# Performance work log

Measured on AMD Instinct MI355X. Metric: run time of the kernel, lower is better.

The kernel has to match this reference:

```python
import jax, jax.numpy as jnp
import numpy as np

EPS = 1e-12

def _normalize(v):
    n = jnp.linalg.norm(v, axis=-1, keepdims=True)
    return v / jnp.maximum(n, EPS)

def _bgs(J):
    # J: [b, N, D, 3, 2] -> rotation matrices R [b, N, D, 3, 3]
    b1 = _normalize(J[..., :, 0])
    a2 = J[..., :, 1]
    dot = jnp.sum(b1 * a2, axis=-1, keepdims=True)
    b2 = _normalize(a2 - dot * b1)
    b3 = jnp.cross(b1, b2)
    return jnp.stack([b1, b2, b3], axis=-1)  # columns b1,b2,b3

def setup_inputs() -> dict:
    key = jax.random.key(0)
    k1, k2, k3, k4, k5 = jax.random.split(key, 5)
    B, N, D, OUT = 16, 4096, 64, 64
    X = jax.random.normal(k1, (B, N, D, 3), dtype=jnp.float32)
    J = jax.random.normal(k2, (B, N, D, 3, 2), dtype=jnp.float32)
    A = jax.random.normal(k3, (OUT, D), dtype=jnp.float32)
    Bm = jax.random.normal(k4, (OUT, D), dtype=jnp.float32)
    C = jax.random.normal(k5, (OUT, D), dtype=jnp.float32)
    return {"X": X, "J": J, "A": A, "Bm": Bm, "C": C}

def reference(X, J, A, Bm, C):
    R = _bgs(J)  # [b, N, D, 3, 3]
    # RT_i . X == column i of R dotted with X -> scalar per channel
    RTX = jnp.einsum('bndij,bndi->bndj', R, X)  # [b, N, D, 3], j-th entry = RT_j X
    rt0 = RTX[..., 0:1]
    rt1 = RTX[..., 1:2]
    rt2 = RTX[..., 2:3]
    col0 = R[..., :, 0]
    col1 = R[..., :, 1]
    col2 = R[..., :, 2]
    # a_term (after adding b_term, as in original forward)
    a_term = col1 * rt1 + col2 * rt2 + col2 * rt1 - col1 * rt2  # [b, N, D, 3]
    c_term = col0 * rt0
    Y = jnp.einsum('fe,bnei->bnfi', A, a_term) + jnp.einsum('fe,bnei->bnfi', C, c_term)
    Y = jnp.einsum('fe,bnei->bnfi', Bm, Y)
    return Y
```

## Files before the change

### kernel.cpp

```cpp
#include <hip/hip_runtime.h>


typedef __bf16 bf16x8 __attribute__((ext_vector_type(8)));
typedef float floatx4 __attribute__((ext_vector_type(4)));

#define RSW 68

__global__ __launch_bounds__(256) void prep_kernel(const float* __restrict__ A,
                                                   const float* __restrict__ Bm,
                                                   const float* __restrict__ C,
                                                   __bf16* __restrict__ acat) {
    int tid = blockIdx.x * 256 + threadIdx.x;
    int f = tid >> 6;
    int e = tid & 63;
    float m = 0.f, m2 = 0.f;
    #pragma unroll 8
    for (int k = 0; k < 64; ++k) {
        float b = Bm[f * 64 + k];
        m  = fmaf(b, A[k * 64 + e], m);
        m2 = fmaf(b, C[k * 64 + e], m2);
    }
    acat[f * 128 + 2 * e]     = (__bf16)m;
    acat[f * 128 + 2 * e + 1] = (__bf16)m2;
}

static __device__ __forceinline__ unsigned pk(float a, float c) {
    unsigned short ua = __builtin_bit_cast(unsigned short, (__bf16)a);
    unsigned short uc = __builtin_bit_cast(unsigned short, (__bf16)c);
    return ((unsigned)uc << 16) | ua;
}

__global__ __launch_bounds__(256, 3) void main_kernel(const float* __restrict__ X,
                                                      const float* __restrict__ J,
                                                      const __bf16* __restrict__ acat,
                                                      float* __restrict__ out) {
    __shared__ __align__(16) float buf[4][3120];

    const int wave = threadIdx.x >> 6;
    const int lane = threadIdx.x & 63;
    const int l15  = lane & 15;
    const int quad = lane >> 4;
    const int pbase = blockIdx.x * 16 + wave * 4;

    float* stg = buf[wave];

    {
        const floatx4* jg = (const floatx4*)(J + (size_t)pbase * 384);
        const floatx4* xg = (const floatx4*)(X + (size_t)pbase * 192);
        floatx4 jt[6], xt[3];
        #pragma unroll
        for (int t = 0; t < 6; ++t) jt[t] = jg[t * 64 + lane];
        #pragma unroll
        for (int t = 0; t < 3; ++t) xt[t] = xg[t * 64 + lane];
        floatx4* sj = (floatx4*)stg;
        floatx4* sx = (floatx4*)(stg + 1536);
        #pragma unroll
        for (int t = 0; t < 6; ++t) sj[t * 64 + lane] = jt[t];
        #pragma unroll
        for (int t = 0; t < 3; ++t) sx[t * 64 + lane] = xt[t];
    }

    __asm__ volatile("s_waitcnt lgkmcnt(0)" ::: "memory");

    unsigned* zw = (unsigned*)(stg + 2304);

    #pragma unroll
    for (int pi = 0; pi < 4; ++pi) {
        const float* jst = stg + pi * 384 + lane * 6;
        float2 ja = *(const float2*)(jst);
        float2 jb = *(const float2*)(jst + 2);
        float2 jc = *(const float2*)(jst + 4);
        const float* xst = stg + 1536 + pi * 192 + lane * 3;
        float xx = xst[0], xy = xst[1], xz = xst[2];

        float a0x = ja.x, a0y = jb.x, a0z = jc.x;
        float a1x = ja.y, a1y = jb.y, a1z = jc.y;

        float n0 = sqrtf(a0x * a0x + a0y * a0y + a0z * a0z);
        float r0 = 1.0f / fmaxf(n0, 1e-12f);
        float b1x = a0x * r0, b1y = a0y * r0, b1z = a0z * r0;

        float d  = b1x * a1x + b1y * a1y + b1z * a1z;
        float ux = a1x - d * b1x, uy = a1y - d * b1y, uz = a1z - d * b1z;
        float n2 = sqrtf(ux * ux + uy * uy + uz * uz);
        float r2 = 1.0f / fmaxf(n2, 1e-12f);
        float b2x = ux * r2, b2y = uy * r2, b2z = uz * r2;

        float b3x = b1y * b2z - b1z * b2y;
        float b3y = b1z * b2x - b1x * b2z;
        float b3z = b1x * b2y - b1y * b2x;

        float rt0 = b1x * xx + b1y * xy + b1z * xz;
        float rt1 = b2x * xx + b2y * xy + b2z * xz;
        float rt2 = b3x * xx + b3y * xy + b3z * xz;

        float s = rt1 - rt2, t = rt1 + rt2;

        unsigned* zr = zw + (pi * 3) * RSW;
        zr[lane]           = pk(b2x * s + b3x * t, b1x * rt0);
        zr[RSW + lane]     = pk(b2y * s + b3y * t, b1y * rt0);
        zr[2 * RSW + lane] = pk(b2z * s + b3z * t, b1z * rt0);
    }

    bf16x8 afrag[4][4];
    #pragma unroll
    for (int mt = 0; mt < 4; ++mt)
        #pragma unroll
        for (int kc = 0; kc < 4; ++kc)
            afrag[mt][kc] = *(const bf16x8*)(acat + (mt * 16 + l15) * 128 + kc * 32 + quad * 8);

    __asm__ volatile("s_waitcnt lgkmcnt(0)" ::: "memory");

    floatx4 acc[4];
    #pragma unroll
    for (int mt = 0; mt < 4; ++mt) acc[mt] = (floatx4){0.f, 0.f, 0.f, 0.f};

    int row = l15 > 11 ? 11 : l15;
    #pragma unroll
    for (int kc = 0; kc < 4; ++kc) {
        bf16x8 b = *(const bf16x8*)((const __bf16*)zw + row * 136 + kc * 32 + quad * 8);
        #pragma unroll
        for (int mt = 0; mt < 4; ++mt)
            acc[mt] = __builtin_amdgcn_mfma_f32_16x16x32_bf16(afrag[mt][kc], b, acc[mt], 0, 0, 0);
    }

    __asm__ volatile("s_waitcnt lgkmcnt(0)" ::: "memory");

    float* dl = stg;
    #pragma unroll
    for (int mt = 0; mt < 4; ++mt) {
        int n = l15;
        if (n < 12) {
            int pl = (n * 21846) >> 16;
            int i  = n - pl * 3;
            float* dst = dl + pl * 196 + i;
            #pragma unroll
            for (int r = 0; r < 4; ++r) {
                int f = mt * 16 + quad * 4 + r;
                dst[f * 3] = acc[mt][r];
            }
        }
    }

    __asm__ volatile("s_waitcnt lgkmcnt(0)" ::: "memory");

    floatx4* og = (floatx4*)(out + (size_t)pbase * 192);
    #pragma unroll
    for (int t = 0; t < 3; ++t) {
        int g  = t * 64 + lane;
        int pg = (g * 1366) >> 16;
        int o  = g - pg * 48;
        og[g] = *(const floatx4*)(dl + pg * 196 + o * 4);
    }
}

extern "C" void kernel_launch(void* const* d_in, const int* in_sizes, int n_in,
                              void* d_out, int out_size, void* d_ws, size_t ws_size,
                              hipStream_t stream) {
    const float* X  = (const float*)d_in[0];
    const float* J  = (const float*)d_in[1];
    const float* A  = (const float*)d_in[2];
    const float* Bm = (const float*)d_in[3];
    const float* C  = (const float*)d_in[4];
    float* out = (float*)d_out;
    __bf16* acat = (__bf16*)d_ws;

    prep_kernel<<<16, 256, 0, stream>>>(A, Bm, C, acat);

    main_kernel<<<4096, 256, 0, stream>>>(X, J, acat, out);
}
```

Before: 209.2 us.

## Use direct global-to-LDS loads, persistent loop over tiles, smaller LDS footprint

Replaces the register-staged global loads of J and X with global_load_lds builtins that write straight into shared memory. The kernel becomes persistent: each wave handles four tiles in a loop, and the grid shrinks by a factor of four, so the B-matrix fragments are loaded once per wave and reused across tiles. Per-wave LDS drops (buffers overlap), which allows four blocks per CU. The risk is that with no prefetch, each iteration's loads are serialized behind the compute, and overlapping the buffers within a wave needs careful ordering.

```diff
diff --git a/kernel.cpp b/kernel.cpp
--- a/kernel.cpp
+++ b/kernel.cpp
@@ -5,6 +5,14 @@
 typedef float floatx4 __attribute__((ext_vector_type(4)));
 
 #define RSW 68
+#define WLDS 2320
+
+typedef const __attribute__((address_space(1))) unsigned guint;
+typedef __attribute__((address_space(3))) unsigned suint;
+
+static __device__ __forceinline__ void load16(const float* g, float* l) {
+    __builtin_amdgcn_global_load_lds((guint*)g, (suint*)l, 16, 0, 0);
+}
 
 __global__ __launch_bounds__(256) void prep_kernel(const float* __restrict__ A,
                                                    const float* __restrict__ Bm,
@@ -30,77 +38,17 @@
     return ((unsigned)uc << 16) | ua;
 }
 
-__global__ __launch_bounds__(256, 3) void main_kernel(const float* __restrict__ X,
+__global__ __launch_bounds__(256, 4) void main_kernel(const float* __restrict__ X,
                                                       const float* __restrict__ J,
                                                       const __bf16* __restrict__ acat,
                                                       float* __restrict__ out) {
-    __shared__ __align__(16) float buf[4][3120];
+    __shared__ __align__(16) float buf[4][WLDS];
 
     const int wave = threadIdx.x >> 6;
     const int lane = threadIdx.x & 63;
     const int l15  = lane & 15;
     const int quad = lane >> 4;
-    const int pbase = blockIdx.x * 16 + wave * 4;
-
     float* stg = buf[wave];
-
-    {
-        const floatx4* jg = (const floatx4*)(J + (size_t)pbase * 384);
-        const floatx4* xg = (const floatx4*)(X + (size_t)pbase * 192);
-        floatx4 jt[6], xt[3];
-        #pragma unroll
-        for (int t = 0; t < 6; ++t) jt[t] = jg[t * 64 + lane];
-        #pragma unroll
-        for (int t = 0; t < 3; ++t) xt[t] = xg[t * 64 + lane];
-        floatx4* sj = (floatx4*)stg;
-        floatx4* sx = (floatx4*)(stg + 1536);
-        #pragma unroll
-        for (int t = 0; t < 6; ++t) sj[t * 64 + lane] = jt[t];
-        #pragma unroll
-        for (int t = 0; t < 3; ++t) sx[t * 64 + lane] = xt[t];
-    }
-
-    __asm__ volatile("s_waitcnt lgkmcnt(0)" ::: "memory");
-
-    unsigned* zw = (unsigned*)(stg + 2304);
-
-    #pragma unroll
-    for (int pi = 0; pi < 4; ++pi) {
-        const float* jst = stg + pi * 384 + lane * 6;
-        float2 ja = *(const float2*)(jst);
-        float2 jb = *(const float2*)(jst + 2);
-        float2 jc = *(const float2*)(jst + 4);
-        const float* xst = stg + 1536 + pi * 192 + lane * 3;
-        float xx = xst[0], xy = xst[1], xz = xst[2];
-
-        float a0x = ja.x, a0y = jb.x, a0z = jc.x;
-        float a1x = ja.y, a1y = jb.y, a1z = jc.y;
-
-        float n0 = sqrtf(a0x * a0x + a0y * a0y + a0z * a0z);
-        float r0 = 1.0f / fmaxf(n0, 1e-12f);
-        float b1x = a0x * r0, b1y = a0y * r0, b1z = a0z * r0;
-
-        float d  = b1x * a1x + b1y * a1y + b1z * a1z;
-        float ux = a1x - d * b1x, uy = a1y - d * b1y, uz = a1z - d * b1z;
-        float n2 = sqrtf(ux * ux + uy * uy + uz * uz);
-        float r2 = 1.0f / fmaxf(n2, 1e-12f);
-        float b2x = ux * r2, b2y = uy * r2, b2z = uz * r2;
-
-        float b3x = b1y * b2z - b1z * b2y;
-        float b3y = b1z * b2x - b1x * b2z;
-        float b3z = b1x * b2y - b1y * b2x;
-
-        float rt0 = b1x * xx + b1y * xy + b1z * xz;
-        float rt1 = b2x * xx + b2y * xy + b2z * xz;
-        float rt2 = b3x * xx + b3y * xy + b3z * xz;
-
-        float s = rt1 - rt2, t = rt1 + rt2;
-
-        unsigned* zr = zw + (pi * 3) * RSW;
-        zr[lane]           = pk(b2x * s + b3x * t, b1x * rt0);
-        zr[RSW + lane]     = pk(b2y * s + b3y * t, b1y * rt0);
-        zr[2 * RSW + lane] = pk(b2z * s + b3z * t, b1z * rt0);
-    }
 
     bf16x8 afrag[4][4];
     #pragma unroll
@@ -109,48 +57,101 @@
         for (int kc = 0; kc < 4; ++kc)
             afrag[mt][kc] = *(const bf16x8*)(acat + (mt * 16 + l15) * 128 + kc * 32 + quad * 8);
 
-    __asm__ volatile("s_waitcnt lgkmcnt(0)" ::: "memory");
+    #pragma unroll 1
+    for (int it = 0; it < 4; ++it) {
+        const int tile = it * 4096 + blockIdx.x * 4 + wave;
+        const size_t pbase = (size_t)tile * 4;
 
-    floatx4 acc[4];
-    #pragma unroll
-    for (int mt = 0; mt < 4; ++mt) acc[mt] = (floatx4){0.f, 0.f, 0.f, 0.f};
+        const float* jg = J + pbase * 384;
+        const float* xg = X + pbase * 192;
+        #pragma unroll
+        for (int t = 0; t < 6; ++t) load16(jg + (t * 64 + lane) * 4, stg + t * 256);
+        #pragma unroll
+        for (int t = 0; t < 3; ++t) load16(xg + (t * 64 + lane) * 4, stg + 1536 + t * 256);
 
-    int row = l15 > 11 ? 11 : l15;
-    #pragma unroll
-    for (int kc = 0; kc < 4; ++kc) {
-        bf16x8 b = *(const bf16x8*)((const __bf16*)zw + row * 136 + kc * 32 + quad * 8);
+        __asm__ volatile("s_waitcnt vmcnt(0)" ::: "memory");
+
+        unsigned* zw = (unsigned*)stg;
+
         #pragma unroll
-        for (int mt = 0; mt < 4; ++mt)
-            acc[mt] = __builtin_amdgcn_mfma_f32_16x16x32_bf16(afrag[mt][kc], b, acc[mt], 0, 0, 0);
-    }
+        for (int pi = 0; pi < 4; ++pi) {
+            const float* jst = stg + pi * 384 + lane * 6;
+            float2 ja = *(const float2*)(jst);
+            float2 jb = *(const float2*)(jst + 2);
+            float2 jc = *(const float2*)(jst + 4);
+            const float* xst = stg + 1536 + pi * 192 + lane * 3;
+            float xx = xst[0], xy = xst[1], xz = xst[2];
 
-    __asm__ volatile("s_waitcnt lgkmcnt(0)" ::: "memory");
+            float a0x = ja.x, a0y = jb.x, a0z = jc.x;
+            float a1x = ja.y, a1y = jb.y, a1z = jc.y;
 
-    float* dl = stg;
-    #pragma unroll
-    for (int mt = 0; mt < 4; ++mt) {
-        int n = l15;
-        if (n < 12) {
-            int pl = (n * 21846) >> 16;
-            int i  = n - pl * 3;
-            float* dst = dl + pl * 196 + i;
+            float n0 = sqrtf(a0x * a0x + a0y * a0y + a0z * a0z);
+            float r0 = 1.0f / fmaxf(n0, 1e-12f);
+            float b1x = a0x * r0, b1y = a0y * r0, b1z = a0z * r0;
+
+            float d  = b1x * a1x + b1y * a1y + b1z * a1z;
+            float ux = a1x - d * b1x, uy = a1y - d * b1y, uz = a1z - d * b1z;
+            float n2 = sqrtf(ux * ux + uy * uy + uz * uz);
+            float r2 = 1.0f / fmaxf(n2, 1e-12f);
+            float b2x = ux * r2, b2y = uy * r2, b2z = uz * r2;
+
+            float b3x = b1y * b2z - b1z * b2y;
+            float b3y = b1z * b2x - b1x * b2z;
+            float b3z = b1x * b2y - b1y * b2x;
+
+            float rt0 = b1x * xx + b1y * xy + b1z * xz;
+            float rt1 = b2x * xx + b2y * xy + b2z * xz;
+            float rt2 = b3x * xx + b3y * xy + b3z * xz;
+
+            float s = rt1 - rt2, t = rt1 + rt2;
+
+            unsigned* zr = zw + (pi * 3) * RSW;
+            zr[lane]           = pk(b2x * s + b3x * t, b1x * rt0);
+            zr[RSW + lane]     = pk(b2y * s + b3y * t, b1y * rt0);
+            zr[2 * RSW + lane] = pk(b2z * s + b3z * t, b1z * rt0);
+        }
+
+        __asm__ volatile("s_waitcnt lgkmcnt(0)" ::: "memory");
+
+        floatx4 acc[4];
+        #pragma unroll
+        for (int mt = 0; mt < 4; ++mt) acc[mt] = (floatx4){0.f, 0.f, 0.f, 0.f};
+
+        int row = l15 > 11 ? 11 : l15;
+        #pragma unroll
+        for (int kc = 0; kc < 4; ++kc) {
+            bf16x8 b = *(const bf16x8*)((const __bf16*)zw + row * 136 + kc * 32 + quad * 8);
             #pragma unroll
-            for (int r = 0; r < 4; ++r) {
-                int f = mt * 16 + quad * 4 + r;
-                dst[f * 3] = acc[mt][r];
+            for (int mt = 0; mt < 4; ++mt)
+                acc[mt] = __builtin_amdgcn_mfma_f32_16x16x32_bf16(afrag[mt][kc], b, acc[mt], 0, 0, 0);
+        }
+
+        float* dl = stg + 832;
+        #pragma unroll
+        for (int mt = 0; mt < 4; ++mt) {
+            int n = l15;
+            if (n < 12) {
+                int pl = (n * 21846) >> 16;
+                int i  = n - pl * 3;
+                float* dst = dl + pl * 196 + i;
+                #pragma unroll
+                for (int r = 0; r < 4; ++r) {
+                    int f = mt * 16 + quad * 4 + r;
+                    dst[f * 3] = acc[mt][r];
+                }
             }
         }
-    }
 
-    __asm__ volatile("s_waitcnt lgkmcnt(0)" ::: "memory");
+        __asm__ volatile("s_waitcnt lgkmcnt(0)" ::: "memory");
 
-    floatx4* og = (floatx4*)(out + (size_t)pbase * 192);
-    #pragma unroll
-    for (int t = 0; t < 3; ++t) {
-        int g  = t * 64 + lane;
-        int pg = (g * 1366) >> 16;
-        int o  = g - pg * 48;
-        og[g] = *(const floatx4*)(dl + pg * 196 + o * 4);
+        floatx4* og = (floatx4*)(out + pbase * 192);
+        #pragma unroll
+        for (int t = 0; t < 3; ++t) {
+            int g  = t * 64 + lane;
+            int pg = (g * 1366) >> 16;
+            int o  = g - pg * 48;
+            og[g] = *(const floatx4*)(dl + pg * 196 + o * 4);
+        }
     }
 }
 
@@ -167,5 +168,5 @@
 
     prep_kernel<<<16, 256, 0, stream>>>(A, Bm, C, acat);
 
-    main_kernel<<<4096, 256, 0, stream>>>(X, J, acat, out);
+    main_kernel<<<1024, 256, 0, stream>>>(X, J, acat, out);
 }
```

New measurement: 212.9 us. No clear change (+1.8%).
